# Optimization experiments

Measured on AMD Instinct MI355X. Metric: run time of the kernel, lower is better.

## Reference

```python
import jax, jax.numpy as jnp
import numpy as np

D_MODEL = 1024
D_STATE = 64
HEADDIM = 64
D_INNER = 2 * D_MODEL          # expand=2 -> 2048
NHEADS = D_INNER // HEADDIM    # 32
D_IN_PROJ = 2 * D_INNER + 2 * D_STATE + NHEADS  # 4256 (ngroups=1)
CHANNELS = D_INNER + 2 * D_STATE                # 2176
KSIZE = 4
LN_EPS = 1e-5


def setup_inputs() -> dict:
    key = jax.random.key(0)
    ks = jax.random.split(key, 8)
    B, L = 2, 2048
    u = jax.random.normal(ks[0], (B, L, D_MODEL), jnp.float32)
    W_in1 = jax.random.normal(ks[1], (D_IN_PROJ, D_MODEL), jnp.float32) * 0.02
    A_log = jnp.log(jax.random.uniform(ks[2], (NHEADS,), jnp.float32, 1.0, 16.0))
    conv_w = jax.random.normal(ks[3], (CHANNELS, CHANNELS, KSIZE), jnp.float32) / np.sqrt(CHANNELS * KSIZE)
    conv_b = jax.random.normal(ks[4], (CHANNELS,), jnp.float32) * 0.01
    prelu_a = jnp.array(0.25, jnp.float32)
    W_in2 = jax.random.normal(ks[5], (D_INNER, D_MODEL), jnp.float32) * 0.02
    W_in3 = jax.random.normal(ks[6], (D_MODEL, D_INNER), jnp.float32) * 0.02
    ln_g = jnp.ones((D_INNER,), jnp.float32)
    ln_b = jnp.zeros((D_INNER,), jnp.float32)
    return {"u": u, "W_in1": W_in1, "A_log": A_log, "conv_w": conv_w, "conv_b": conv_b,
            "prelu_a": prelu_a, "W_in2": W_in2, "W_in3": W_in3, "ln_g": ln_g, "ln_b": ln_b}


def _segsum(x):
    # x: (..., T) -> (..., T, T), lower-triangular segment sums, -inf above diag
    T = x.shape[-1]
    cs = jnp.cumsum(x, axis=-1)
    seg = cs[..., :, None] - cs[..., None, :]
    mask = jnp.tril(jnp.ones((T, T), bool))
    return jnp.where(mask, seg, -jnp.inf)


def _ssd(X, A, B, C, block_len):
    # X:(b,L,h,p)  A:(b,L,h)  B,C:(b,L,n)  (ngroups=1, group axis squeezed)
    b, Lseq, h, p = X.shape
    c = Lseq // block_len
    X = X.reshape(b, c, block_len, h, p)
    A = A.reshape(b, c, block_len, h).transpose(0, 3, 1, 2)      # (b,h,c,l)
    B = B.reshape(b, c, block_len, -1)                            # (b,c,l,n)
    C = C.reshape(b, c, block_len, -1)
    A_cumsum = jnp.cumsum(A, axis=-1)                             # (b,h,c,l)
    Lmat = jnp.exp(_segsum(A))                                    # (b,h,c,l,l)
    Y_diag = jnp.einsum('bcln,bcsn,bhcls,bcshp->bclhp', C, B, Lmat, X)
    decay_states = jnp.exp(A_cumsum[..., -1:] - A_cumsum)         # (b,h,c,l)
    states = jnp.einsum('bcln,bhcl,bclhp->bchpn', B, decay_states, X)
    init = jnp.zeros_like(states[:, :1])
    states = jnp.concatenate([init, states], axis=1)              # (b,c+1,h,p,n)
    A_last = jnp.pad(A_cumsum[..., -1], ((0, 0), (0, 0), (1, 0)))
    decay_chunk = jnp.exp(_segsum(A_last))                        # (b,h,c+1,c+1)
    new_states = jnp.einsum('bhzc,bchpn->bzhpn', decay_chunk, states)
    states_off, final_state = new_states[:, :-1], new_states[:, -1]
    state_decay_out = jnp.exp(A_cumsum)
    Y_off = jnp.einsum('bcln,bchpn,bhcl->bclhp', C, states_off, state_decay_out)
    Y = (Y_diag + Y_off).reshape(b, Lseq, h, p)
    return Y, final_state


def reference(u, W_in1, A_log, conv_w, conv_b, prelu_a, W_in2, W_in3, ln_g, ln_b):
    Bsz, L, _ = u.shape
    zxbcdt = u @ W_in1.T                                          # (B,L,4256); d_nonssm=0
    A = -jnp.exp(A_log)
    z = zxbcdt[..., :D_INNER]                                     # split but unused (as in source)
    xBC = zxbcdt[..., D_INNER:D_INNER + CHANNELS]
    dt = zxbcdt[..., D_INNER + CHANNELS:]
    dt_safe = jnp.where(dt <= 20.0, dt, 0.0)
    dt = jnp.where(dt <= 20.0, jnp.log1p(jnp.exp(dt_safe)), dt)   # softplus w/ overflow guard
    A_t = dt * A[None, None, :]                                   # (B,L,H)
    # causal conv (left-pad k-1) + PReLU
    xt = xBC.transpose(0, 2, 1)                                   # (B,C,L)
    conv = jax.lax.conv_general_dilated(xt, conv_w, (1,), [(KSIZE - 1, 0)],
                                        dimension_numbers=('NCH', 'OIH', 'NCH'))
    conv = conv + conv_b[None, :, None]
    conv = jnp.maximum(conv, 0) + prelu_a * jnp.minimum(conv, 0)
    xBC_conv = conv.transpose(0, 2, 1)                            # (B,L,C)
    x = xBC_conv[..., :D_INNER].reshape(Bsz, L, NHEADS, HEADDIM)
    Bmat = xBC_conv[..., D_INNER:D_INNER + D_STATE]
    Cmat = xBC_conv[..., D_INNER + D_STATE:]
    Y, _ = _ssd(x, A_t, Bmat, Cmat, L // 4)
    out = Y.reshape(Bsz, L, D_INNER)
    u2 = jax.nn.gelu(u @ W_in2.T, approximate=False)
    h = u2 * out
    mu = jnp.mean(h, axis=-1, keepdims=True)
    var = jnp.mean((h - mu) ** 2, axis=-1, keepdims=True)
    hn = (h - mu) / jnp.sqrt(var + LN_EPS) * ln_g + ln_b
    return hn @ W_in3.T
```

## Files before the change

### kernel.cpp

```cpp
#include <hip/hip_runtime.h>
#include <stdint.h>

typedef unsigned short u16;
typedef _Float16 f16x8 __attribute__((ext_vector_type(8)));
typedef float f32x4 __attribute__((ext_vector_type(4)));

#define AS1C const __attribute__((address_space(1))) void*
#define AS3P __attribute__((address_space(3))) void*

#define DM 1024
#define DI 2048
#define CHN 2176
#define ROWS 4096
#define PADR_U 2051

__device__ __forceinline__ float h2f(u16 v) {
    union { u16 u; _Float16 h; } x; x.u = v; return (float)x.h;
}
__device__ __forceinline__ u16 f2h(float f) {
    union { _Float16 h; u16 u; } x; x.h = (_Float16)f; return x.u;
}

template<int ASRC, int EPI, int TERMS>
__global__ __launch_bounds__(256) void split_gemm(
    const u16* __restrict__ Ah, const u16* __restrict__ Al,
    const u16* __restrict__ Bh,
    float* __restrict__ Cf, float* __restrict__ Bm, float* __restrict__ Cm,
    u16* __restrict__ Oh,
    int K, int ldA, int ldB, int ldC, int aoffR,
    const float* __restrict__ bias, const float* __restrict__ prelu)
{
    __shared__ u16 Ash[128 * 64];
    __shared__ u16 Asl[TERMS == 2 ? 128 * 64 : 64];
    __shared__ u16 Bsh[128 * 64];
    const int tid = threadIdx.x;
    const int bm = blockIdx.x * 128;
    const int bn = blockIdx.y * 128;
    const int lane = tid & 63;
    const int w = tid >> 6, wr = w >> 1, wc = w & 1;
    const int lrow = lane & 15;
    const int cb = lane >> 4;
    const int trow = tid >> 3;
    const int tcolS = (((tid & 7) ^ (trow & 7)) << 3);

    f32x4 acc[4][4];
#pragma unroll
    for (int m = 0; m < 4; ++m)
#pragma unroll
        for (int n = 0; n < 4; ++n) acc[m][n] = f32x4{0.f, 0.f, 0.f, 0.f};

    for (int k0 = 0; k0 < K; k0 += 64) {
#pragma unroll
        for (int ch = 0; ch < 4; ++ch) {
            long aoff;
            if (ASRC == 1) {
                int kc = k0 >> 10;
                int i0 = k0 & 1023;
                int r = bm + ch * 32 + trow;
                long srow = (long)(r >> 11) * PADR_U + (r & 2047) + kc + aoffR;
                aoff = srow * 1024 + i0 + tcolS;
            } else {
                int r = bm + ch * 32 + trow;
                aoff = (long)r * ldA + k0 + tcolS;
            }
            __builtin_amdgcn_global_load_lds((AS1C)(Ah + aoff), (AS3P)(&Ash[ch * 2048 + tid * 8]), 16, 0, 0);
            if constexpr (TERMS == 2)
                __builtin_amdgcn_global_load_lds((AS1C)(Al + aoff), (AS3P)(&Asl[ch * 2048 + tid * 8]), 16, 0, 0);
            int rr = bn + ch * 32 + trow;
            long boff = (long)rr * ldB + k0 + tcolS;
            __builtin_amdgcn_global_load_lds((AS1C)(Bh + boff), (AS3P)(&Bsh[ch * 2048 + tid * 8]), 16, 0, 0);
        }
        __syncthreads();
#pragma unroll
        for (int kk = 0; kk < 64; kk += 32) {
            const int swz = ((((kk >> 3) + cb) ^ (lrow & 7)) << 3);
            f16x8 ah[4], al[4], bh[4];
#pragma unroll
            for (int m = 0; m < 4; ++m) {
                int o = (wr * 64 + m * 16 + lrow) * 64 + swz;
                ah[m] = *(const f16x8*)&Ash[o];
                if constexpr (TERMS == 2) al[m] = *(const f16x8*)&Asl[o];
            }
#pragma unroll
            for (int n = 0; n < 4; ++n)
                bh[n] = *(const f16x8*)&Bsh[(wc * 64 + n * 16 + lrow) * 64 + swz];
#pragma unroll
            for (int m = 0; m < 4; ++m)
#pragma unroll
                for (int n = 0; n < 4; ++n) {
                    acc[m][n] = __builtin_amdgcn_mfma_f32_16x16x32_f16(ah[m], bh[n], acc[m][n], 0, 0, 0);
                    if constexpr (TERMS == 2)
                        acc[m][n] = __builtin_amdgcn_mfma_f32_16x16x32_f16(al[m], bh[n], acc[m][n], 0, 0, 0);
                }
        }
        __syncthreads();
    }

    float pa = 0.f;
    if (EPI == 2) pa = *prelu;
#pragma unroll
    for (int m = 0; m < 4; ++m) {
#pragma unroll
        for (int n = 0; n < 4; ++n) {
            int col = bn + wc * 64 + n * 16 + lrow;
            int rbase = bm + wr * 64 + m * 16 + ((lane >> 4) << 2);
            float bv = (EPI == 2) ? bias[col] : 0.f;
#pragma unroll
            for (int j = 0; j < 4; ++j) {
                int r = rbase + j;
                float v = acc[m][n][j];
                if (EPI == 0) {
                    Cf[(long)r * ldC + col] = v;
                } else if (EPI == 3) {
                    int kc = r / CHN;
                    int o = r - kc * CHN;
                    Oh[(long)o * 4096 + kc * 1024 + col] = f2h(v);
                } else {
                    v += bv;
                    v = v > 0.f ? v : pa * v;
                    if (col < DI) Cf[(long)r * DI + col] = v;
                    else if (col < DI + 64) Bm[r * 64 + (col - DI)] = v;
                    else Cm[r * 64 + (col - DI - 64)] = v;
                }
            }
        }
    }
}

__global__ void conv_w_split(const float* __restrict__ w,
                             u16* __restrict__ ch_, u16* __restrict__ cl_) {
    int idx = blockIdx.x * 256 + threadIdx.x;
    if (idx < CHN * CHN) {
        int o = idx / CHN, i = idx - o * CHN;
        f32x4 v = *(const f32x4*)&w[(long)idx * 4];
#pragma unroll
        for (int kc = 0; kc < 4; ++kc) {
            long m = (long)(kc * CHN + o) * CHN + i;
            u16 hi = f2h(v[kc]);
            ch_[m] = hi;
            cl_[m] = f2h(v[kc] - h2f(hi));
        }
    }
}

__global__ __launch_bounds__(256) void w1x_t(
    const float* __restrict__ W1, u16* __restrict__ th)
{
    __shared__ float tile[32][33];
    int i0 = blockIdx.x * 32, d0 = blockIdx.y * 32;
    int ti = threadIdx.x & 31, tj = threadIdx.x >> 5;
#pragma unroll
    for (int rr = 0; rr < 32; rr += 8)
        tile[tj + rr][ti] = W1[(long)(2048 + i0 + tj + rr) * 1024 + d0 + ti];
    __syncthreads();
#pragma unroll
    for (int rr = 0; rr < 32; rr += 8)
        th[(long)(d0 + tj + rr) * CHN + i0 + ti] = f2h(tile[ti][tj + rr]);
}

__global__ void u_pad_f16(const float* __restrict__ u, u16* __restrict__ ph) {
    int idx = blockIdx.x * 256 + threadIdx.x;
    if (idx >= 2 * PADR_U * 256) return;
    int row = idx >> 8, c4 = (idx & 255) << 2;
    int b = row >= PADR_U ? 1 : 0;
    int lr = row - b * PADR_U;
    ushort4 h = {0, 0, 0, 0};
    if (lr >= 3) {
        f32x4 v = *(const f32x4*)&u[((long)(b * 2048 + lr - 3)) * 1024 + c4];
        h.x = f2h(v[0]); h.y = f2h(v[1]); h.z = f2h(v[2]); h.w = f2h(v[3]);
    }
    *(ushort4*)&ph[(long)idx * 4] = h;
}

__global__ void cast_f16(const float* __restrict__ in, u16* __restrict__ oh, int n4) {
    int idx = blockIdx.x * 256 + threadIdx.x;
    if (idx < n4) {
        f32x4 v = *(const f32x4*)&in[(long)idx * 4];
        ushort4 h;
        h.x = f2h(v[0]); h.y = f2h(v[1]); h.z = f2h(v[2]); h.w = f2h(v[3]);
        *(ushort4*)&oh[(long)idx * 4] = h;
    }
}

__global__ __launch_bounds__(256) void dt_kernel(
    const float* __restrict__ u, const float* __restrict__ W1,
    const float* __restrict__ A_log, float* __restrict__ A_t)
{
    __shared__ float us[8][1024];
    int r0 = blockIdx.x * 8;
    int tid = threadIdx.x;
#pragma unroll
    for (int rep = 0; rep < 8; ++rep) {
        int idx = rep * 256 + tid;
        int i = idx >> 8, kx = (idx & 255) << 2;
        *(f32x4*)&us[i][kx] = *(const f32x4*)&u[(long)(r0 + i) * 1024 + kx];
    }
    __syncthreads();
    int row = tid >> 5;
    int hh = tid & 31;
    const float* wrow = W1 + (long)(4224 + hh) * 1024;
    f32x4 a4 = {0.f, 0.f, 0.f, 0.f};
#pragma unroll 4
    for (int k = 0; k < 1024; k += 4) {
        f32x4 a = *(const f32x4*)&us[row][k];
        f32x4 b = *(const f32x4*)&wrow[k];
        a4 += a * b;
    }
    float dt = a4[0] + a4[1] + a4[2] + a4[3];
    if (dt <= 20.f) dt = log1pf(__expf(dt));
    float At = dt * (-__expf(A_log[hh]));
    int r = r0 + row;
    int b = r >> 11, l = r & 2047;
    A_t[((long)(b * 32 + hh)) * 2048 + l] = At;
}

__global__ __launch_bounds__(64) void csum_chunk(float* A_t, float* __restrict__ Atot)
{
    int bid = blockIdx.x;
    int lane = threadIdx.x;
    float* p = A_t + (long)bid * 128;
    float v0 = p[lane * 2], v1 = p[lane * 2 + 1];
    float s = v0 + v1;
    float t = s;
#pragma unroll
    for (int d = 1; d < 64; d <<= 1) {
        float o = __shfl_up(t, d);
        if (lane >= d) t += o;
    }
    float excl = t - s;
    p[lane * 2] = excl + v0;
    p[lane * 2 + 1] = excl + s;
    if (lane == 63) Atot[bid] = t;
}

__global__ __launch_bounds__(256) void g_chunk(
    const float* __restrict__ Cm, const float* __restrict__ Bm, float* __restrict__ G)
{
    __shared__ float CsT[128 * 33];
    __shared__ float BsT[128 * 33];
    const int bid = blockIdx.x;
    const int b = bid >> 4, c = bid & 15;
    const long rowbase = (long)b * 2048 + c * 128;
    const int tid = threadIdx.x;
    const int li = tid & 15, si = tid >> 4;
    const int l0 = li * 8, s0 = si * 8;
    float acc[8][8];
#pragma unroll
    for (int i = 0; i < 8; ++i)
#pragma unroll
        for (int j = 0; j < 8; ++j) acc[i][j] = 0.f;

    for (int kt = 0; kt < 2; ++kt) {
        __syncthreads();
#pragma unroll
        for (int t = 0; t < 16; ++t) {
            int idx = t * 256 + tid;
            int row = idx >> 5, k = idx & 31;
            CsT[row * 33 + k] = Cm[(rowbase + row) * 64 + kt * 32 + k];
            BsT[row * 33 + k] = Bm[(rowbase + row) * 64 + kt * 32 + k];
        }
        __syncthreads();
        for (int k = 0; k < 32; ++k) {
            float cv[8], bv[8];
#pragma unroll
            for (int i = 0; i < 8; ++i) cv[i] = CsT[(l0 + i) * 33 + k];
#pragma unroll
            for (int j = 0; j < 8; ++j) bv[j] = BsT[(s0 + j) * 33 + k];
#pragma unroll
            for (int i = 0; i < 8; ++i)
#pragma unroll
                for (int j = 0; j < 8; ++j) acc[i][j] += cv[i] * bv[j];
        }
    }
    float* gz = G + (long)bid * 16384;
#pragma unroll
    for (int i = 0; i < 8; ++i) {
        f32x4 o0 = {acc[i][0], acc[i][1], acc[i][2], acc[i][3]};
        f32x4 o1 = {acc[i][4], acc[i][5], acc[i][6], acc[i][7]};
        *(f32x4*)&gz[(l0 + i) * 128 + s0] = o0;
        *(f32x4*)&gz[(l0 + i) * 128 + s0 + 4] = o1;
    }
}

__global__ __launch_bounds__(256) void ssd_diag_states(
    float* XY, const float* __restrict__ Bm, const float* __restrict__ G,
    const float* __restrict__ cs, const float* __restrict__ Atot, float* __restrict__ Sc)
{
    __shared__ float Xs[128 * 64];
    __shared__ float Gb[32 * 132];
    __shared__ float csL[128];
    __shared__ float dsL[128];
    const int bid = blockIdx.x;
    const int bh = bid >> 4, c = bid & 15;
    const int b = bh >> 5, h = bh & 31;
    const long rowbase = (long)b * 2048 + c * 128;
    const float* gz = G + (long)(b * 16 + c) * 16384;
    const float atot = Atot[bid];
    const int tid = threadIdx.x;

    if (tid < 128) csL[tid] = cs[(long)bh * 2048 + c * 128 + tid];
#pragma unroll
    for (int t = 0; t < 8; ++t) {
        int idx = t * 256 + tid;
        int row = idx >> 4, c4 = (idx & 15) << 2;
        *(f32x4*)&Xs[row * 64 + c4] = *(const f32x4*)&XY[(rowbase + row) * 2048 + h * 64 + c4];
    }
    __syncthreads();
    if (tid < 128) dsL[tid] = __expf(atot - csL[tid]);

    const int lg = tid & 31, pg = tid >> 5;
    const int l0 = lg * 4, p0 = pg * 8;
    float cl[4];
#pragma unroll
    for (int i = 0; i < 4; ++i) cl[i] = csL[l0 + i];
    float acc1[4][8];
#pragma unroll
    for (int i = 0; i < 4; ++i)
#pragma unroll
        for (int j = 0; j < 8; ++j) acc1[i][j] = 0.f;

    for (int st = 0; st < 4; ++st) {
        __syncthreads();
#pragma unroll
        for (int t = 0; t < 16; ++t) {
            int idx = t * 256 + tid;
            int l = idx >> 5, sq = idx & 31;
            Gb[sq * 132 + l] = gz[l * 128 + st * 32 + sq];
        }
        __syncthreads();
        for (int sq = 0; sq < 32; ++sq) {
            int s = st * 32 + sq;
            float css = csL[s];
            f32x4 x0 = *(const f32x4*)&Xs[s * 64 + p0];
            f32x4 x1 = *(const f32x4*)&Xs[s * 64 + p0 + 4];
#pragma unroll
            for (int i = 0; i < 4; ++i) {
                int l = l0 + i;
                float P = (s <= l) ? Gb[sq * 132 + l] * __expf(cl[i] - css) : 0.f;
                acc1[i][0] += P * x0[0]; acc1[i][1] += P * x0[1];
                acc1[i][2] += P * x0[2]; acc1[i][3] += P * x0[3];
                acc1[i][4] += P * x1[0]; acc1[i][5] += P * x1[1];
                acc1[i][6] += P * x1[2]; acc1[i][7] += P * x1[3];
            }
        }
    }

    const int pq = tid & 15, nq = tid >> 4;
    const int pp0 = pq * 4, nn0 = nq * 4;
    float acc2[4][4];
#pragma unroll
    for (int i = 0; i < 4; ++i)
#pragma unroll
        for (int j = 0; j < 4; ++j) acc2[i][j] = 0.f;
    for (int half = 0; half < 2; ++half) {
        __syncthreads();
#pragma unroll
        for (int t = 0; t < 4; ++t) {
            int idx = t * 256 + tid;
            int srow = idx >> 4, c4 = (idx & 15) << 2;
            *(f32x4*)&Gb[srow * 64 + c4] = *(const f32x4*)&Bm[(rowbase + half * 64 + srow) * 64 + c4];
        }
        __syncthreads();
        for (int ss = 0; ss < 64; ++ss) {
            int s = half * 64 + ss;
            float d = dsL[s];
            f32x4 xv = *(const f32x4*)&Xs[s * 64 + pp0];
            f32x4 bv = *(const f32x4*)&Gb[ss * 64 + nn0];
            float xd[4];
#pragma unroll
            for (int i = 0; i < 4; ++i) xd[i] = xv[i] * d;
#pragma unroll
            for (int i = 0; i < 4; ++i)
#pragma unroll
                for (int j = 0; j < 4; ++j) acc2[i][j] += xd[i] * bv[j];
        }
    }
    long scb = (long)bid * 4096;
#pragma unroll
    for (int i = 0; i < 4; ++i) {
        f32x4 o = {acc2[i][0], acc2[i][1], acc2[i][2], acc2[i][3]};
        *(f32x4*)&Sc[scb + (pp0 + i) * 64 + nn0] = o;
    }
#pragma unroll
    for (int i = 0; i < 4; ++i) {
        f32x4 y0 = {acc1[i][0], acc1[i][1], acc1[i][2], acc1[i][3]};
        f32x4 y1 = {acc1[i][4], acc1[i][5], acc1[i][6], acc1[i][7]};
        long yo = (rowbase + l0 + i) * 2048 + h * 64 + p0;
        *(f32x4*)&XY[yo] = y0;
        *(f32x4*)&XY[yo + 4] = y1;
    }
}

__global__ __launch_bounds__(256) void ssd_combine(float* Sc, const float* __restrict__ Atot)
{
    int bh = blockIdx.x;
    int tid = threadIdx.x;
    float run[16];
#pragma unroll
    for (int t = 0; t < 16; ++t) run[t] = 0.f;
    for (int c = 0; c < 16; ++c) {
        float e = __expf(Atot[bh * 16 + c]);
        long base = (long)(bh * 16 + c) * 4096;
#pragma unroll
        for (int t = 0; t < 16; ++t) {
            long idx = base + t * 256 + tid;
            float tmp = Sc[idx];
            Sc[idx] = run[t];
            run[t] = e * run[t] + tmp;
        }
    }
}

__global__ __launch_bounds__(256) void ssd_yoff(
    const float* __restrict__ Cm, const float* __restrict__ Sin,
    const float* __restrict__ cs, float* XY)
{
    __shared__ float Cs[128 * 66];
    __shared__ float St[64 * 68];
    __shared__ float csL[128];
    const int bid = blockIdx.x;
    const int bh = bid >> 4, c = bid & 15;
    const int b = bh >> 5, h = bh & 31;
    const long rowbase = (long)b * 2048 + c * 128;
    const int tid = threadIdx.x;

    if (tid < 128) csL[tid] = cs[(long)bh * 2048 + c * 128 + tid];
#pragma unroll
    for (int t = 0; t < 32; ++t) {
        int idx = t * 256 + tid;
        int row = idx >> 6, n = idx & 63;
        Cs[row * 66 + n] = Cm[(rowbase + row) * 64 + n];
    }
#pragma unroll
    for (int t = 0; t < 16; ++t) {
        int idx = t * 256 + tid;
        int p = idx >> 6, n = idx & 63;
        St[n * 68 + p] = Sin[(long)bid * 4096 + p * 64 + n];
    }
    __syncthreads();

    const int lg = tid & 31, pg = tid >> 5;
    const int l0 = lg * 4, p0 = pg * 8;
    float el[4];
#pragma unroll
    for (int i = 0; i < 4; ++i) el[i] = __expf(csL[l0 + i]);
    float acc[4][8];
#pragma unroll
    for (int i = 0; i < 4; ++i)
#pragma unroll
        for (int j = 0; j < 8; ++j) acc[i][j] = 0.f;

    for (int n = 0; n < 64; ++n) {
        float cv[4];
#pragma unroll
        for (int i = 0; i < 4; ++i) cv[i] = Cs[(l0 + i) * 66 + n];
        f32x4 s0 = *(const f32x4*)&St[n * 68 + p0];
        f32x4 s1 = *(const f32x4*)&St[n * 68 + p0 + 4];
#pragma unroll
        for (int i = 0; i < 4; ++i) {
            acc[i][0] += cv[i] * s0[0]; acc[i][1] += cv[i] * s0[1];
            acc[i][2] += cv[i] * s0[2]; acc[i][3] += cv[i] * s0[3];
            acc[i][4] += cv[i] * s1[0]; acc[i][5] += cv[i] * s1[1];
            acc[i][6] += cv[i] * s1[2]; acc[i][7] += cv[i] * s1[3];
        }
    }
#pragma unroll
    for (int i = 0; i < 4; ++i) {
        long yo = (rowbase + l0 + i) * 2048 + h * 64 + p0;
        f32x4 y0 = *(const f32x4*)&XY[yo];
        f32x4 y1 = *(const f32x4*)&XY[yo + 4];
        y0[0] += el[i] * acc[i][0]; y0[1] += el[i] * acc[i][1];
        y0[2] += el[i] * acc[i][2]; y0[3] += el[i] * acc[i][3];
        y1[0] += el[i] * acc[i][4]; y1[1] += el[i] * acc[i][5];
        y1[2] += el[i] * acc[i][6]; y1[3] += el[i] * acc[i][7];
        *(f32x4*)&XY[yo] = y0;
        *(f32x4*)&XY[yo + 4] = y1;
    }
}

__global__ __launch_bounds__(256) void ln_kernel(
    const float* __restrict__ u2raw, const float* __restrict__ Y,
    const float* __restrict__ lng, const float* __restrict__ lnb,
    u16* __restrict__ hh)
{
    __shared__ float hbuf[2048];
    __shared__ float rs[4], rs2[4];
    int r = blockIdx.x;
    int tid = threadIdx.x;
    float s = 0.f, s2 = 0.f;
    for (int j = tid; j < 2048; j += 256) {
        float x = u2raw[(long)r * 2048 + j];
        float g = 0.5f * x * (1.f + erff(x * 0.70710678118654752f));
        float hv = g * Y[(long)r * 2048 + j];
        hbuf[j] = hv;
        s += hv;
        s2 += hv * hv;
    }
    for (int d = 32; d > 0; d >>= 1) {
        s += __shfl_down(s, d);
        s2 += __shfl_down(s2, d);
    }
    if ((tid & 63) == 0) { rs[tid >> 6] = s; rs2[tid >> 6] = s2; }
    __syncthreads();
    float tot = rs[0] + rs[1] + rs[2] + rs[3];
    float tot2 = rs2[0] + rs2[1] + rs2[2] + rs2[3];
    float mu = tot * (1.f / 2048.f);
    float var = tot2 * (1.f / 2048.f) - mu * mu;
    float inv = rsqrtf(var + 1e-5f);
    for (int j = tid; j < 2048; j += 256) {
        float v = (hbuf[j] - mu) * inv * lng[j] + lnb[j];
        hh[(long)r * 2048 + j] = f2h(v);
    }
}

extern "C" void kernel_launch(void* const* d_in, const int* in_sizes, int n_in,
                              void* d_out, int out_size, void* d_ws, size_t ws_size,
                              hipStream_t stream) {
    const float* u = (const float*)d_in[0];
    const float* W1 = (const float*)d_in[1];
    const float* A_log = (const float*)d_in[2];
    const float* convw = (const float*)d_in[3];
    const float* convb = (const float*)d_in[4];
    const float* prelu = (const float*)d_in[5];
    const float* W2 = (const float*)d_in[6];
    const float* W3 = (const float*)d_in[7];
    const float* lng = (const float*)d_in[8];
    const float* lnb = (const float*)d_in[9];
    float* out = (float*)d_out;

    char* base = (char*)d_ws;
    size_t off = 0;
    auto nxt = [&](size_t bytes) -> char* {
        char* r = base + off;
        off = (off + bytes + 255) & ~(size_t)255;
        return r;
    };
    u16* cw_h = (u16*)nxt((size_t)4 * CHN * CHN * 2);
    u16* cw_l = (u16*)nxt((size_t)4 * CHN * CHN * 2);
    float* u2raw = (float*)cw_h;
    u16* hn_h = cw_l;
    u16* up_h = (u16*)nxt((size_t)2 * PADR_U * 1024 * 2);
    u16* w1t_h = (u16*)nxt((size_t)1024 * CHN * 2);
    float* Gbuf = (float*)w1t_h;
    u16* wbig_h = (u16*)nxt((size_t)CHN * 4096 * 2);
    u16* w2_h = (u16*)nxt((size_t)DI * DM * 2);
    u16* w3_h = (u16*)nxt((size_t)DM * DI * 2);
    float* A_t = (float*)nxt((size_t)64 * 2048 * 4);
    float* Atot = (float*)nxt((size_t)64 * 16 * 4);
    float* XY = (float*)nxt((size_t)ROWS * DI * 4);
    float* Bmat = (float*)nxt((size_t)ROWS * 64 * 4);
    float* Cmat = (float*)nxt((size_t)ROWS * 64 * 4);
    float* Sc = (float*)nxt((size_t)64 * 16 * 4096 * 4);

    conv_w_split<<<(CHN * CHN + 255) / 256, 256, 0, stream>>>(convw, cw_h, cw_l);
    w1x_t<<<dim3(68, 32), 256, 0, stream>>>(W1, w1t_h);
    u_pad_f16<<<(2 * PADR_U * 256 + 255) / 256, 256, 0, stream>>>(u, up_h);
    cast_f16<<<DI * DM / 1024, 256, 0, stream>>>(W2, w2_h, DI * DM / 4);
    cast_f16<<<DM * DI / 1024, 256, 0, stream>>>(W3, w3_h, DM * DI / 4);
    dt_kernel<<<512, 256, 0, stream>>>(u, W1, A_log, A_t);
    csum_chunk<<<1024, 64, 0, stream>>>(A_t, Atot);

    split_gemm<0, 3, 2><<<dim3(68, 8), 256, 0, stream>>>(
        cw_h, cw_l, w1t_h, nullptr, nullptr, nullptr, wbig_h,
        2176, 2176, 2176, 0, 0, nullptr, nullptr);

    split_gemm<1, 2, 1><<<dim3(32, 17), 256, 0, stream>>>(
        up_h, nullptr, wbig_h, XY, Bmat, Cmat, nullptr,
        4096, 0, 4096, 0, 0, convb, prelu);

    split_gemm<1, 0, 1><<<dim3(32, 16), 256, 0, stream>>>(
        up_h, nullptr, w2_h, u2raw, nullptr, nullptr, nullptr,
        1024, 0, 1024, 2048, 3, nullptr, nullptr);

    g_chunk<<<32, 256, 0, stream>>>(Cmat, Bmat, Gbuf);
    ssd_diag_states<<<1024, 256, 0, stream>>>(XY, Bmat, Gbuf, A_t, Atot, Sc);
    ssd_combine<<<64, 256, 0, stream>>>(Sc, Atot);
    ssd_yoff<<<1024, 256, 0, stream>>>(Cmat, Sc, A_t, XY);

    ln_kernel<<<4096, 256, 0, stream>>>(u2raw, XY, lng, lnb, hn_h);

    split_gemm<0, 0, 1><<<dim3(32, 8), 256, 0, stream>>>(
        hn_h, nullptr, w3_h, out, nullptr, nullptr, nullptr,
        2048, 2048, 2048, 1024, 0, nullptr, nullptr);
}
```

Baseline: 561.5 us.

## Drop low-half conv weight split, fuse conv and W2 GEMMs, widen ssd_combine

The conv-weight fold GEMM now uses only the high fp16 half of the conv weights, so the second operand and its MFMA pass are gone. The conv GEMM and the u@W2 GEMM are merged into one launch (conv_g2) that picks its weights, K and epilogue from blockIdx.y. ssd_combine is split across four blocks per head, giving more parallelism. Dropping the low-order weight term lowers precision of the folded conv weights, which risks accuracy loss.

```diff
diff --git a/kernel.cpp b/kernel.cpp
--- a/kernel.cpp
+++ b/kernel.cpp
@@ -21,14 +21,12 @@
     union { _Float16 h; u16 u; } x; x.h = (_Float16)f; return x.u;
 }
 
-template<int ASRC, int EPI, int TERMS>
+template<int EPI, int TERMS>
 __global__ __launch_bounds__(256) void split_gemm(
     const u16* __restrict__ Ah, const u16* __restrict__ Al,
     const u16* __restrict__ Bh,
-    float* __restrict__ Cf, float* __restrict__ Bm, float* __restrict__ Cm,
-    u16* __restrict__ Oh,
-    int K, int ldA, int ldB, int ldC, int aoffR,
-    const float* __restrict__ bias, const float* __restrict__ prelu)
+    float* __restrict__ Cf, u16* __restrict__ Oh,
+    int K, int ldA, int ldB, int ldC)
 {
     __shared__ u16 Ash[128 * 64];
     __shared__ u16 Asl[TERMS == 2 ? 128 * 64 : 64];
@@ -52,17 +50,8 @@
     for (int k0 = 0; k0 < K; k0 += 64) {
 #pragma unroll
         for (int ch = 0; ch < 4; ++ch) {
-            long aoff;
-            if (ASRC == 1) {
-                int kc = k0 >> 10;
-                int i0 = k0 & 1023;
-                int r = bm + ch * 32 + trow;
-                long srow = (long)(r >> 11) * PADR_U + (r & 2047) + kc + aoffR;
-                aoff = srow * 1024 + i0 + tcolS;
-            } else {
-                int r = bm + ch * 32 + trow;
-                aoff = (long)r * ldA + k0 + tcolS;
-            }
+            int r = bm + ch * 32 + trow;
+            long aoff = (long)r * ldA + k0 + tcolS;
             __builtin_amdgcn_global_load_lds((AS1C)(Ah + aoff), (AS3P)(&Ash[ch * 2048 + tid * 8]), 16, 0, 0);
             if constexpr (TERMS == 2)
                 __builtin_amdgcn_global_load_lds((AS1C)(Al + aoff), (AS3P)(&Asl[ch * 2048 + tid * 8]), 16, 0, 0);
@@ -96,50 +85,124 @@
         __syncthreads();
     }
 
-    float pa = 0.f;
-    if (EPI == 2) pa = *prelu;
 #pragma unroll
     for (int m = 0; m < 4; ++m) {
 #pragma unroll
         for (int n = 0; n < 4; ++n) {
             int col = bn + wc * 64 + n * 16 + lrow;
             int rbase = bm + wr * 64 + m * 16 + ((lane >> 4) << 2);
-            float bv = (EPI == 2) ? bias[col] : 0.f;
 #pragma unroll
             for (int j = 0; j < 4; ++j) {
                 int r = rbase + j;
                 float v = acc[m][n][j];
                 if (EPI == 0) {
                     Cf[(long)r * ldC + col] = v;
-                } else if (EPI == 3) {
+                } else {
                     int kc = r / CHN;
                     int o = r - kc * CHN;
                     Oh[(long)o * 4096 + kc * 1024 + col] = f2h(v);
-                } else {
+                }
+            }
+        }
+    }
+}
+
+__global__ __launch_bounds__(256) void conv_g2(
+    const u16* __restrict__ up, const u16* __restrict__ Wbig, const u16* __restrict__ W2,
+    float* __restrict__ Xf, float* __restrict__ Bm, float* __restrict__ Cm,
+    float* __restrict__ u2raw,
+    const float* __restrict__ bias, const float* __restrict__ prelu)
+{
+    __shared__ u16 Ash[128 * 64];
+    __shared__ u16 Bsh[128 * 64];
+    const int tid = threadIdx.x;
+    const bool isconv = blockIdx.y < 17;
+    const u16* __restrict__ Bmat = isconv ? Wbig : W2;
+    const int K = isconv ? 4096 : 1024;
+    const int ldB = K;
+    const int aoffR = isconv ? 0 : 3;
+    const int bm = blockIdx.x * 128;
+    const int bn = (isconv ? blockIdx.y : blockIdx.y - 17) * 128;
+    const int lane = tid & 63;
+    const int w = tid >> 6, wr = w >> 1, wc = w & 1;
+    const int lrow = lane & 15;
+    const int cb = lane >> 4;
+    const int trow = tid >> 3;
+    const int tcolS = (((tid & 7) ^ (trow & 7)) << 3);
+
+    f32x4 acc[4][4];
+#pragma unroll
+    for (int m = 0; m < 4; ++m)
+#pragma unroll
+        for (int n = 0; n < 4; ++n) acc[m][n] = f32x4{0.f, 0.f, 0.f, 0.f};
+
+    for (int k0 = 0; k0 < K; k0 += 64) {
+        const int kc = k0 >> 10;
+        const int i0 = k0 & 1023;
+#pragma unroll
+        for (int ch = 0; ch < 4; ++ch) {
+            int r = bm + ch * 32 + trow;
+            long srow = (long)(r >> 11) * PADR_U + (r & 2047) + kc + aoffR;
+            long aoff = srow * 1024 + i0 + tcolS;
+            __builtin_amdgcn_global_load_lds((AS1C)(up + aoff), (AS3P)(&Ash[ch * 2048 + tid * 8]), 16, 0, 0);
+            int rr = bn + ch * 32 + trow;
+            long boff = (long)rr * ldB + k0 + tcolS;
+            __builtin_amdgcn_global_load_lds((AS1C)(Bmat + boff), (AS3P)(&Bsh[ch * 2048 + tid * 8]), 16, 0, 0);
+        }
+        __syncthreads();
+#pragma unroll
+        for (int kk = 0; kk < 64; kk += 32) {
+            const int swz = ((((kk >> 3) + cb) ^ (lrow & 7)) << 3);
+            f16x8 a[4], b[4];
+#pragma unroll
+            for (int m = 0; m < 4; ++m)
+                a[m] = *(const f16x8*)&Ash[(wr * 64 + m * 16 + lrow) * 64 + swz];
+#pragma unroll
+            for (int n = 0; n < 4; ++n)
+                b[n] = *(const f16x8*)&Bsh[(wc * 64 + n * 16 + lrow) * 64 + swz];
+#pragma unroll
+            for (int m = 0; m < 4; ++m)
+#pragma unroll
+                for (int n = 0; n < 4; ++n)
+                    acc[m][n] = __builtin_amdgcn_mfma_f32_16x16x32_f16(a[m], b[n], acc[m][n], 0, 0, 0);
+        }
+        __syncthreads();
+    }
+
+    const float pa = isconv ? *prelu : 0.f;
+#pragma unroll
+    for (int m = 0; m < 4; ++m) {
+#pragma unroll
+        for (int n = 0; n < 4; ++n) {
+            int col = bn + wc * 64 + n * 16 + lrow;
+            int rbase = bm + wr * 64 + m * 16 + ((lane >> 4) << 2);
+            float bv = isconv ? bias[col] : 0.f;
+#pragma unroll
+            for (int j = 0; j < 4; ++j) {
+                int r = rbase + j;
+                float v = acc[m][n][j];
+                if (isconv) {
                     v += bv;
                     v = v > 0.f ? v : pa * v;
-                    if (col < DI) Cf[(long)r * DI + col] = v;
+                    if (col < DI) Xf[(long)r * DI + col] = v;
                     else if (col < DI + 64) Bm[r * 64 + (col - DI)] = v;
                     else Cm[r * 64 + (col - DI - 64)] = v;
+                } else {
+                    u2raw[(long)r * 2048 + col] = v;
                 }
             }
         }
     }
 }
 
-__global__ void conv_w_split(const float* __restrict__ w,
-                             u16* __restrict__ ch_, u16* __restrict__ cl_) {
+__global__ void conv_w_h(const float* __restrict__ w, u16* __restrict__ ch_) {
     int idx = blockIdx.x * 256 + threadIdx.x;
     if (idx < CHN * CHN) {
         int o = idx / CHN, i = idx - o * CHN;
         f32x4 v = *(const f32x4*)&w[(long)idx * 4];
 #pragma unroll
-        for (int kc = 0; kc < 4; ++kc) {
-            long m = (long)(kc * CHN + o) * CHN + i;
-            u16 hi = f2h(v[kc]);
-            ch_[m] = hi;
-            cl_[m] = f2h(v[kc] - h2f(hi));
-        }
+        for (int kc = 0; kc < 4; ++kc)
+            ch_[(long)(kc * CHN + o) * CHN + i] = f2h(v[kc]);
     }
 }
 
@@ -393,16 +456,17 @@
 
 __global__ __launch_bounds__(256) void ssd_combine(float* Sc, const float* __restrict__ Atot)
 {
-    int bh = blockIdx.x;
+    int bh = blockIdx.x >> 2;
+    int q = blockIdx.x & 3;
     int tid = threadIdx.x;
-    float run[16];
-#pragma unroll
-    for (int t = 0; t < 16; ++t) run[t] = 0.f;
+    float run[4];
+#pragma unroll
+    for (int t = 0; t < 4; ++t) run[t] = 0.f;
     for (int c = 0; c < 16; ++c) {
         float e = __expf(Atot[bh * 16 + c]);
-        long base = (long)(bh * 16 + c) * 4096;
-#pragma unroll
-        for (int t = 0; t < 16; ++t) {
+        long base = (long)(bh * 16 + c) * 4096 + q * 1024;
+#pragma unroll
+        for (int t = 0; t < 4; ++t) {
             long idx = base + t * 256 + tid;
             float tmp = Sc[idx];
             Sc[idx] = run[t];
@@ -536,9 +600,8 @@
         return r;
     };
     u16* cw_h = (u16*)nxt((size_t)4 * CHN * CHN * 2);
-    u16* cw_l = (u16*)nxt((size_t)4 * CHN * CHN * 2);
     float* u2raw = (float*)cw_h;
-    u16* hn_h = cw_l;
+    u16* hn_h = (u16*)nxt((size_t)ROWS * DI * 2);
     u16* up_h = (u16*)nxt((size_t)2 * PADR_U * 1024 * 2);
     u16* w1t_h = (u16*)nxt((size_t)1024 * CHN * 2);
     float* Gbuf = (float*)w1t_h;
@@ -552,7 +615,7 @@
     float* Cmat = (float*)nxt((size_t)ROWS * 64 * 4);
     float* Sc = (float*)nxt((size_t)64 * 16 * 4096 * 4);
 
-    conv_w_split<<<(CHN * CHN + 255) / 256, 256, 0, stream>>>(convw, cw_h, cw_l);
+    conv_w_h<<<(CHN * CHN + 255) / 256, 256, 0, stream>>>(convw, cw_h);
     w1x_t<<<dim3(68, 32), 256, 0, stream>>>(W1, w1t_h);
     u_pad_f16<<<(2 * PADR_U * 256 + 255) / 256, 256, 0, stream>>>(u, up_h);
     cast_f16<<<DI * DM / 1024, 256, 0, stream>>>(W2, w2_h, DI * DM / 4);
@@ -560,26 +623,19 @@
     dt_kernel<<<512, 256, 0, stream>>>(u, W1, A_log, A_t);
     csum_chunk<<<1024, 64, 0, stream>>>(A_t, Atot);
 
-    split_gemm<0, 3, 2><<<dim3(68, 8), 256, 0, stream>>>(
-        cw_h, cw_l, w1t_h, nullptr, nullptr, nullptr, wbig_h,
-        2176, 2176, 2176, 0, 0, nullptr, nullptr);
-
-    split_gemm<1, 2, 1><<<dim3(32, 17), 256, 0, stream>>>(
-        up_h, nullptr, wbig_h, XY, Bmat, Cmat, nullptr,
-        4096, 0, 4096, 0, 0, convb, prelu);
-
-    split_gemm<1, 0, 1><<<dim3(32, 16), 256, 0, stream>>>(
-        up_h, nullptr, w2_h, u2raw, nullptr, nullptr, nullptr,
-        1024, 0, 1024, 2048, 3, nullptr, nullptr);
+    split_gemm<3, 1><<<dim3(68, 8), 256, 0, stream>>>(
+        cw_h, nullptr, w1t_h, nullptr, wbig_h, 2176, 2176, 2176, 0);
+
+    conv_g2<<<dim3(32, 33), 256, 0, stream>>>(
+        up_h, wbig_h, w2_h, XY, Bmat, Cmat, u2raw, convb, prelu);
 
     g_chunk<<<32, 256, 0, stream>>>(Cmat, Bmat, Gbuf);
     ssd_diag_states<<<1024, 256, 0, stream>>>(XY, Bmat, Gbuf, A_t, Atot, Sc);
-    ssd_combine<<<64, 256, 0, stream>>>(Sc, Atot);
+    ssd_combine<<<256, 256, 0, stream>>>(Sc, Atot);
     ssd_yoff<<<1024, 256, 0, stream>>>(Cmat, Sc, A_t, XY);
 
     ln_kernel<<<4096, 256, 0, stream>>>(u2raw, XY, lng, lnb, hn_h);
 
-    split_gemm<0, 0, 1><<<dim3(32, 8), 256, 0, stream>>>(
-        hn_h, nullptr, w3_h, out, nullptr, nullptr, nullptr,
-        2048, 2048, 2048, 1024, 0, nullptr, nullptr);
-}
+    split_gemm<0, 1><<<dim3(32, 8), 256, 0, stream>>>(
+        hn_h, nullptr, w3_h, out, nullptr, 2048, 2048, 2048, 1024);
+}
```

After: 532.8 us. 1.05x faster.
